# Kernel optimization log

Hardware: AMD Instinct MI355X
Metric: run time of the kernel (lower is better)

Reference implementation:

```python
import jax, jax.numpy as jnp
import numpy as np

VOCAB, BLOCK, C, H, L = 65, 60, 384, 6, 6
HS = C // H  # 64
EPS = 1e-5


def _ln(x, g, b):
    mu = jnp.mean(x, axis=-1, keepdims=True)
    var = jnp.mean(jnp.square(x - mu), axis=-1, keepdims=True)
    return (x - mu) * jax.lax.rsqrt(var + EPS) * g + b


def setup_inputs() -> dict:
    key = jax.random.key(0)
    ks = jax.random.split(key, 16)
    std = 0.02
    B, T = 2048, 60
    inp = {
        'context': jax.random.randint(ks[0], (B, T), 0, VOCAB),
        'tok_emb': std * jax.random.normal(ks[1], (VOCAB, C), jnp.float32),
        'pos_emb': std * jax.random.normal(ks[2], (BLOCK, C), jnp.float32),
        # per-head projections stacked: [L, H, C, HS]
        'wq': std * jax.random.normal(ks[3], (L, H, C, HS), jnp.float32),
        'wk': std * jax.random.normal(ks[4], (L, H, C, HS), jnp.float32),
        'wv': std * jax.random.normal(ks[5], (L, H, C, HS), jnp.float32),
        'wo': std * jax.random.normal(ks[6], (L, C, C), jnp.float32),
        'bo': jnp.zeros((L, C), jnp.float32),
        'ln1_g': jnp.ones((L, C), jnp.float32),
        'ln1_b': jnp.zeros((L, C), jnp.float32),
        'ln2_g': jnp.ones((L, C), jnp.float32),
        'ln2_b': jnp.zeros((L, C), jnp.float32),
        'w1': std * jax.random.normal(ks[7], (L, C, 4 * C), jnp.float32),
        'b1': jnp.zeros((L, 4 * C), jnp.float32),
        'w2': std * jax.random.normal(ks[8], (L, 4 * C, C), jnp.float32),
        'b2': jnp.zeros((L, C), jnp.float32),
        'lnf_g': jnp.ones((C,), jnp.float32),
        'lnf_b': jnp.zeros((C,), jnp.float32),
        'lm_w': std * jax.random.normal(ks[9], (C, VOCAB), jnp.float32),
        'lm_b': jnp.zeros((VOCAB,), jnp.float32),
    }
    return inp


def _forward(context, tok_emb, pos_emb, wq, wk, wv, wo, bo,
             ln1_g, ln1_b, ln2_g, ln2_b, w1, b1, w2, b2,
             lnf_g, lnf_b, lm_w, lm_b):
    B, T = context.shape
    x = tok_emb[context] + pos_emb[:T]  # [B,T,C]
    causal = jnp.tril(jnp.ones((T, T), bool))
    neg_inf = jnp.finfo(x.dtype).min

    def block(x, p):
        (wq_l, wk_l, wv_l, wo_l, bo_l, g1, b1n, g2, b2n, w1_l, bb1, w2_l, bb2) = p
        h = _ln(x, g1, b1n)
        q = jnp.einsum('btc,hcd->bhtd', h, wq_l)
        k = jnp.einsum('btc,hcd->bhtd', h, wk_l)
        v = jnp.einsum('btc,hcd->bhtd', h, wv_l)
        scores = jnp.einsum('bhtd,bhsd->bhts', q, k) * (HS ** -0.5)
        scores = jnp.where(causal, scores, neg_inf)
        probs = jax.nn.softmax(scores, axis=-1)
        o = jnp.einsum('bhts,bhsd->bhtd', probs, v)
        o = o.transpose(0, 2, 1, 3).reshape(B, T, C)  # concat heads
        x = x + o @ wo_l + bo_l
        h = _ln(x, g2, b2n)
        x = x + jax.nn.relu(h @ w1_l + bb1) @ w2_l + bb2
        return x, None

    params = (wq, wk, wv, wo, bo, ln1_g, ln1_b, ln2_g, ln2_b, w1, b1, w2, b2)
    x, _ = jax.lax.scan(block, x, params)
    x = _ln(x, lnf_g, lnf_b)
    return x @ lm_w + lm_b  # [B,T,VOCAB]


def reference(context, tok_emb, pos_emb, wq, wk, wv, wo, bo,
              ln1_g, ln1_b, ln2_g, ln2_b, w1, b1, w2, b2,
              lnf_g, lnf_b, lm_w, lm_b):
    return _forward(context, tok_emb, pos_emb, wq, wk, wv, wo, bo,
                    ln1_g, ln1_b, ln2_g, ln2_b, w1, b1, w2, b2,
                    lnf_g, lnf_b, lm_w, lm_b)
```

## Files before the change

### kernel.cpp

```cpp
#include <hip/hip_runtime.h>


#define B_  2048
#define T_  60
#define C_  384
#define H_  6
#define HS_ 64
#define L_  6
#define FF_ 1536
#define V_  65

typedef unsigned int  u32;
typedef unsigned short u16;
typedef short bf16x8 __attribute__((ext_vector_type(8)));
typedef float f32x4  __attribute__((ext_vector_type(4)));

__device__ __forceinline__ float bf2f(u32 u) {
  return __uint_as_float(u << 16);
}
__device__ __forceinline__ u16 f2bf(float f) {
  u32 u = __float_as_uint(f);
  u = u + 0x7FFFu + ((u >> 16) & 1u);
  return (u16)(u >> 16);
}

typedef const __attribute__((address_space(1))) unsigned int gas_u32;
typedef __attribute__((address_space(3))) unsigned int las_u32;
__device__ __forceinline__ void gload16(const u16* g, u16* l) {
  __builtin_amdgcn_global_load_lds((gas_u32*)g, (las_u32*)l, 16, 0, 0);
}

__global__ void tconv_k(const float* __restrict__ src, u16* __restrict__ dst,
                        int K, int N, long srcStride, int nH, long sL, long sH)
{
  __shared__ float t[32][33];
  int z = blockIdx.z;
  int l = z / nH, hh = z % nH;
  const float* s = src + (long)z * srcStride;
  u16* d = dst + l * sL + hh * sH;
  int n0 = blockIdx.x * 32, k0 = blockIdx.y * 32;
  for (int yy = threadIdx.y; yy < 32; yy += 8) {
    int k = k0 + yy, n = n0 + threadIdx.x;
    t[yy][threadIdx.x] = (k < K && n < N) ? s[(long)k * N + n] : 0.f;
  }
  __syncthreads();
  for (int yy = threadIdx.y; yy < 32; yy += 8) {
    int n = n0 + yy, k = k0 + threadIdx.x;
    if (n < N && k < K) d[(long)n * K + k] = f2bf(t[threadIdx.x][yy]);
  }
}

__global__ __launch_bounds__(256) void embed_k(const int* __restrict__ ctx,
    const float* __restrict__ tok, const float* __restrict__ pos,
    float* __restrict__ x)
{
  int idx = blockIdx.x * 256 + threadIdx.x;
  int row = idx / (C_ / 4);
  int c   = (idx % (C_ / 4)) * 4;
  int t   = row % T_;
  int tk  = ctx[row];
  float4 a = *(const float4*)(tok + (long)tk * C_ + c);
  float4 p = *(const float4*)(pos + (long)t  * C_ + c);
  float4 o = make_float4(a.x + p.x, a.y + p.y, a.z + p.z, a.w + p.w);
  *(float4*)(x + (long)idx * 4) = o;
}

__global__ __launch_bounds__(256) void ln_k(const float* __restrict__ x,
    const float* __restrict__ g, const float* __restrict__ b,
    u16* __restrict__ h)
{
  int lane = threadIdx.x & 63;
  int wv   = threadIdx.x >> 6;
  long row = (long)blockIdx.x * 4 + wv;
  const float* xr = x + row * C_;
  int c0 = lane * 6;
  float v0[6];
  #pragma unroll
  for (int i = 0; i < 6; i++) v0[i] = xr[c0 + i];
  float s = 0.f, sq = 0.f;
  #pragma unroll
  for (int i = 0; i < 6; i++) { s += v0[i]; sq += v0[i] * v0[i]; }
  #pragma unroll
  for (int off = 32; off > 0; off >>= 1) {
    s  += __shfl_xor(s,  off, 64);
    sq += __shfl_xor(sq, off, 64);
  }
  float mu  = s * (1.f / C_);
  float var = sq * (1.f / C_) - mu * mu;
  float rs  = rsqrtf(var + 1e-5f);
  u16* hr = h + row * C_;
  #pragma unroll
  for (int i = 0; i < 6; i++) {
    float hv = (v0[i] - mu) * rs * g[c0 + i] + b[c0 + i];
    hr[c0 + i] = f2bf(hv);
  }
}

template<int RELU, int RES, int OBF>
__global__ __launch_bounds__(512) void gemm128g(const u16* __restrict__ A,
    const u16* __restrict__ Wt, const float* __restrict__ bias,
    const float* __restrict__ resid, void* __restrict__ outp,
    int N, int K, int mT, int nT)
{
  __shared__ __align__(16) u16 As[2][128][4][8];
  __shared__ __align__(16) u16 Bs[2][128][4][8];
  int tid = threadIdx.x;
  int bid = blockIdx.x;
  int mtile, ntile;
  if ((mT & 7) == 0) {
    int xcd = bid & 7, loc = bid >> 3;
    int q = loc / nT;
    mtile = xcd * (mT >> 3) + q;
    ntile = loc - q * nT;
  } else {
    int q = bid / nT;
    mtile = q;
    ntile = bid - q * nT;
  }
  long mBase = (long)mtile * 128;
  int  nBase = ntile * 128;
  int lane = tid & 63, wv = tid >> 6;
  int l15 = lane & 15, l4 = lane >> 4;
  int wr = wv >> 1, wc = wv & 1;
  int srow = tid >> 2;
  int seg  = (tid & 3) ^ ((tid >> 4) & 3);
  const u16* aL = A  + (mBase + srow) * (long)K + seg * 8;
  const u16* bL = Wt + ((long)nBase + srow) * K + seg * 8;
  u16* aD0 = &As[0][wv << 4][0][0];
  u16* bD0 = &Bs[0][wv << 4][0][0];
  u16* aD1 = &As[1][wv << 4][0][0];
  u16* bD1 = &Bs[1][wv << 4][0][0];
  int swR = l4 ^ (l15 >> 2);

  f32x4 acc[2][4];
  #pragma unroll
  for (int i = 0; i < 2; i++)
    #pragma unroll
    for (int j = 0; j < 4; j++)
      acc[i][j] = (f32x4){0.f, 0.f, 0.f, 0.f};

  gload16(aL, aD0);
  gload16(bL, bD0);
  __syncthreads();

  int cur = 0;
  for (int k0 = 0; k0 < K; k0 += 32) {
    if (k0 + 32 < K) {
      gload16(aL + k0 + 32, cur ? aD0 : aD1);
      gload16(bL + k0 + 32, cur ? bD0 : bD1);
    }
    bf16x8 af[2], bfr[4];
    #pragma unroll
    for (int i = 0; i < 2; i++)
      af[i] = *(const bf16x8*)&As[cur][wr * 32 + i * 16 + l15][swR][0];
    #pragma unroll
    for (int j = 0; j < 4; j++)
      bfr[j] = *(const bf16x8*)&Bs[cur][wc * 64 + j * 16 + l15][swR][0];
    #pragma unroll
    for (int i = 0; i < 2; i++)
      #pragma unroll
      for (int j = 0; j < 4; j++)
        acc[i][j] = __builtin_amdgcn_mfma_f32_16x16x32_bf16(
            af[i], bfr[j], acc[i][j], 0, 0, 0);
    __syncthreads();
    cur ^= 1;
  }

  #pragma unroll
  for (int i = 0; i < 2; i++) {
    #pragma unroll
    for (int j = 0; j < 4; j++) {
      int n = nBase + wc * 64 + j * 16 + l15;
      float bv = bias ? bias[n] : 0.f;
      #pragma unroll
      for (int r = 0; r < 4; r++) {
        long row = mBase + wr * 32 + i * 16 + l4 * 4 + r;
        float vv = acc[i][j][r] + bv;
        if (RELU) vv = fmaxf(vv, 0.f);
        if (RES)  vv += resid[row * N + n];
        if (OBF) ((u16*)outp)[row * N + n] = f2bf(vv);
        else     ((float*)outp)[row * N + n] = vv;
      }
    }
  }
}

template<int OBF>
__global__ __launch_bounds__(256) void gemm_head(const u16* __restrict__ A,
    const u16* __restrict__ Wt, const float* __restrict__ bias,
    void* __restrict__ outp, int N, int K)
{
  __shared__ __align__(16) u16 As[128][4][8];
  __shared__ __align__(16) u16 Bs[64][4][8];
  int tid  = threadIdx.x;
  int nt   = blockIdx.x;
  int nBase = nt * 64;
  long mBase = (long)blockIdx.y * 128;
  int lane = tid & 63, wv = tid >> 6;
  int l15 = lane & 15, l4 = lane >> 4;
  int sseg = tid & 3;
  int srow = tid >> 2;
  int swW = sseg ^ ((srow >> 2) & 3);
  int swR = l4 ^ (l15 >> 2);
  const u16* a0p = A + (mBase + srow) * K + sseg * 8;
  const u16* a1p = a0p + (long)64 * K;
  bool colOK = (nBase + srow) < N;
  const u16* bp  = Wt + (long)(nBase + srow) * K + sseg * 8;

  f32x4 acc[2][4];
  #pragma unroll
  for (int i = 0; i < 2; i++)
    #pragma unroll
    for (int j = 0; j < 4; j++)
      acc[i][j] = (f32x4){0.f, 0.f, 0.f, 0.f};

  for (int k0 = 0; k0 < K; k0 += 32) {
    uint4 av0 = *(const uint4*)(a0p + k0);
    uint4 av1 = *(const uint4*)(a1p + k0);
    uint4 bv  = colOK ? *(const uint4*)(bp + k0) : make_uint4(0, 0, 0, 0);
    *(uint4*)&As[srow][swW][0]      = av0;
    *(uint4*)&As[srow + 64][swW][0] = av1;
    *(uint4*)&Bs[srow][swW][0]      = bv;
    __syncthreads();
    bf16x8 af[2], bfr[4];
    af[0] = *(const bf16x8*)&As[wv * 32 + l15][swR][0];
    af[1] = *(const bf16x8*)&As[wv * 32 + 16 + l15][swR][0];
    #pragma unroll
    for (int j = 0; j < 4; j++)
      bfr[j] = *(const bf16x8*)&Bs[j * 16 + l15][swR][0];
    #pragma unroll
    for (int i = 0; i < 2; i++)
      #pragma unroll
      for (int j = 0; j < 4; j++)
        acc[i][j] = __builtin_amdgcn_mfma_f32_16x16x32_bf16(
            af[i], bfr[j], acc[i][j], 0, 0, 0);
    __syncthreads();
  }

  #pragma unroll
  for (int i = 0; i < 2; i++) {
    #pragma unroll
    for (int j = 0; j < 4; j++) {
      int n = nBase + j * 16 + l15;
      if (n < N) {
        #pragma unroll
        for (int r = 0; r < 4; r++) {
          long row = mBase + wv * 32 + i * 16 + l4 * 4 + r;
          float vv = acc[i][j][r];
          if (bias) vv += bias[n];
          if (OBF) ((u16*)outp)[row * N + n] = f2bf(vv);
          else     ((float*)outp)[row * N + n] = vv;
        }
      }
    }
  }
}

__global__ __launch_bounds__(256) void attn_k(const u16* __restrict__ qkv,
    u16* __restrict__ ao)
{
  __shared__ __align__(16) u16 qs[64][72];
  __shared__ __align__(16) u16 ks[64][72];
  __shared__ __align__(16) u16 vT[64][72];
  __shared__ __align__(16) u16 ps[64][72];
  int tid = threadIdx.x;
  int bb = blockIdx.x / H_;
  int hh = blockIdx.x % H_;
  const u16* base = qkv + ((long)bb * T_) * 1152 + hh * HS_;

  for (int i = tid; i < 576; i += 256)
    ((uint4*)vT)[i] = make_uint4(0, 0, 0, 0);
  __syncthreads();

  for (int i = tid; i < 480; i += 256) {
    int t = i >> 3, d0 = (i & 7) << 3;
    const u16* rp = base + (long)t * 1152;
    *(uint4*)&qs[t][d0] = *(const uint4*)(rp + d0);
    *(uint4*)&ks[t][d0] = *(const uint4*)(rp + 384 + d0);
    uint4 rv = *(const uint4*)(rp + 768 + d0);
    u16 vv[8] = {(u16)(rv.x & 0xffffu), (u16)(rv.x >> 16),
                 (u16)(rv.y & 0xffffu), (u16)(rv.y >> 16),
                 (u16)(rv.z & 0xffffu), (u16)(rv.z >> 16),
                 (u16)(rv.w & 0xffffu), (u16)(rv.w >> 16)};
    #pragma unroll
    for (int m = 0; m < 8; m++) vT[d0 + m][t] = vv[m];
  }
  __syncthreads();

  int lane = tid & 63, wv = tid >> 6;
  int l15 = lane & 15, quad = lane >> 4;

  bf16x8 aq0 = *(const bf16x8*)&qs[wv * 16 + l15][quad * 8];
  bf16x8 aq1 = *(const bf16x8*)&qs[wv * 16 + l15][32 + quad * 8];
  f32x4 s[4];
  #pragma unroll
  for (int jt = 0; jt < 4; jt++) {
    bf16x8 b0 = *(const bf16x8*)&ks[jt * 16 + l15][quad * 8];
    bf16x8 b1 = *(const bf16x8*)&ks[jt * 16 + l15][32 + quad * 8];
    f32x4 a2 = (f32x4){0.f, 0.f, 0.f, 0.f};
    a2 = __builtin_amdgcn_mfma_f32_16x16x32_bf16(aq0, b0, a2, 0, 0, 0);
    a2 = __builtin_amdgcn_mfma_f32_16x16x32_bf16(aq1, b1, a2, 0, 0, 0);
    s[jt] = a2;
  }

  int rbase = wv * 16 + quad * 4;
  #pragma unroll
  for (int r = 0; r < 4; r++) {
    int row = rbase + r;
    float v0[4];
    #pragma unroll
    for (int jt = 0; jt < 4; jt++) {
      int col = jt * 16 + l15;
      float sv = s[jt][r] * 0.125f;
      v0[jt] = (col <= row) ? sv : -1e30f;
    }
    float m = fmaxf(fmaxf(v0[0], v0[1]), fmaxf(v0[2], v0[3]));
    #pragma unroll
    for (int off = 1; off < 16; off <<= 1) m = fmaxf(m, __shfl_xor(m, off, 64));
    float sum = 0.f;
    #pragma unroll
    for (int jt = 0; jt < 4; jt++) { v0[jt] = __expf(v0[jt] - m); sum += v0[jt]; }
    #pragma unroll
    for (int off = 1; off < 16; off <<= 1) sum += __shfl_xor(sum, off, 64);
    float inv = 1.f / sum;
    #pragma unroll
    for (int jt = 0; jt < 4; jt++)
      ps[row][jt * 16 + l15] = f2bf(v0[jt] * inv);
  }
  __syncthreads();

  bf16x8 ap0 = *(const bf16x8*)&ps[wv * 16 + l15][quad * 8];
  bf16x8 ap1 = *(const bf16x8*)&ps[wv * 16 + l15][32 + quad * 8];
  long obase = ((long)bb * T_) * C_ + hh * HS_;
  #pragma unroll
  for (int dt = 0; dt < 4; dt++) {
    bf16x8 b0 = *(const bf16x8*)&vT[dt * 16 + l15][quad * 8];
    bf16x8 b1 = *(const bf16x8*)&vT[dt * 16 + l15][32 + quad * 8];
    f32x4 a2 = (f32x4){0.f, 0.f, 0.f, 0.f};
    a2 = __builtin_amdgcn_mfma_f32_16x16x32_bf16(ap0, b0, a2, 0, 0, 0);
    a2 = __builtin_amdgcn_mfma_f32_16x16x32_bf16(ap1, b1, a2, 0, 0, 0);
    #pragma unroll
    for (int r = 0; r < 4; r++) {
      int row = rbase + r;
      if (row < T_)
        ao[obase + (long)row * C_ + dt * 16 + l15] = f2bf(a2[r]);
    }
  }
}

extern "C" void kernel_launch(void* const* d_in, const int* in_sizes, int n_in,
                              void* d_out, int out_size, void* d_ws, size_t ws_size,
                              hipStream_t stream)
{
  const int*   ctx  = (const int*)  d_in[0];
  const float* tok  = (const float*)d_in[1];
  const float* pos  = (const float*)d_in[2];
  const float* wq   = (const float*)d_in[3];
  const float* wk   = (const float*)d_in[4];
  const float* wv   = (const float*)d_in[5];
  const float* wo   = (const float*)d_in[6];
  const float* bo   = (const float*)d_in[7];
  const float* ln1g = (const float*)d_in[8];
  const float* ln1b = (const float*)d_in[9];
  const float* ln2g = (const float*)d_in[10];
  const float* ln2b = (const float*)d_in[11];
  const float* w1   = (const float*)d_in[12];
  const float* b1   = (const float*)d_in[13];
  const float* w2   = (const float*)d_in[14];
  const float* b2   = (const float*)d_in[15];
  const float* lnfg = (const float*)d_in[16];
  const float* lnfb = (const float*)d_in[17];
  const float* lmw  = (const float*)d_in[18];
  const float* lmb  = (const float*)d_in[19];
  float* out = (float*)d_out;

  const long nQKV = (long)L_ * H_ * C_ * HS_;
  const long nWO  = (long)L_ * C_ * C_;
  const long nW1  = (long)L_ * C_ * FF_;
  const long nLM  = (long)C_ * V_;
  u16* wqkvT = (u16*)d_ws;
  u16* woT = wqkvT + 3 * nQKV;
  u16* w1T = woT + nWO;
  u16* w2T = w1T + nW1;
  u16* lmT = w2T + nW1;
  const size_t wbytes = (size_t)(nQKV * 3 + nWO + nW1 * 2 + nLM) * 2;

  int chunkB = 32;
  {
    const int cand[] = {256, 128, 64, 32};
    for (int i = 0; i < 4; i++) {
      size_t U = (size_t)cand[i] * T_ * C_ * 2;
      if (wbytes + 7 * U <= ws_size) { chunkB = cand[i]; break; }
    }
  }
  const long BTc = (long)chunkB * T_;
  char* wsb = (char*)d_ws + wbytes;
  const size_t U = (size_t)BTc * C_ * 2;
  float* x    = (float*)wsb;
  u16*   h    = (u16*)(wsb + 2 * U);
  char*  reg  = wsb + 3 * U;
  u16* qkvb = (u16*)reg;
  u16* ab   = (u16*)(reg + 3 * U);
  u16* fb   = (u16*)reg;

  {
    dim3 tb(32, 8);
    const long sL = 1152L * 384, sH = 64L * 384, sec = 384L * 384;
    tconv_k<<<dim3(2, 12, L_ * H_), tb, 0, stream>>>(wq, wqkvT,
        C_, HS_, (long)C_ * HS_, H_, sL, sH);
    tconv_k<<<dim3(2, 12, L_ * H_), tb, 0, stream>>>(wk, wqkvT + sec,
        C_, HS_, (long)C_ * HS_, H_, sL, sH);
    tconv_k<<<dim3(2, 12, L_ * H_), tb, 0, stream>>>(wv, wqkvT + 2 * sec,
        C_, HS_, (long)C_ * HS_, H_, sL, sH);
    tconv_k<<<dim3(12, 12, L_), tb, 0, stream>>>(wo, woT,
        C_, C_, (long)C_ * C_, 1, (long)C_ * C_, 0);
    tconv_k<<<dim3(48, 12, L_), tb, 0, stream>>>(w1, w1T,
        C_, FF_, (long)C_ * FF_, 1, (long)C_ * FF_, 0);
    tconv_k<<<dim3(12, 48, L_), tb, 0, stream>>>(w2, w2T,
        FF_, C_, (long)FF_ * C_, 1, (long)FF_ * C_, 0);
    tconv_k<<<dim3(3, 12, 1), tb, 0, stream>>>(lmw, lmT,
        C_, V_, (long)C_ * V_, 1, 0, 0);
  }

  const long qkvL = 1152L * 384;
  const long woL  = (long)C_ * C_;
  const long w1L  = (long)C_ * FF_;
  dim3 blk(256);
  dim3 blk5(512);
  dim3 gEmb((u32)(BTc * C_ / 4 / 256));
  dim3 gLN((u32)(BTc / 4));
  int mT = (int)(BTc / 128);
  dim3 gHd(2, (u32)(BTc / 128));
  dim3 gAt((u32)(chunkB * H_));

  for (int c0 = 0; c0 < B_; c0 += chunkB) {
    const long tok0 = (long)c0 * T_;
    const int* ctxc = ctx + tok0;
    float* outc = out + tok0 * V_;

    embed_k<<<gEmb, blk, 0, stream>>>(ctxc, tok, pos, x);

    for (int l = 0; l < L_; l++) {
      ln_k<<<gLN, blk, 0, stream>>>(x, ln1g + l * C_, ln1b + l * C_, h);
      gemm128g<0,0,1><<<dim3(mT * 9), blk5, 0, stream>>>(h, wqkvT + l * qkvL,
          nullptr, nullptr, qkvb, 1152, C_, mT, 9);
      attn_k<<<gAt, blk, 0, stream>>>(qkvb, ab);
      gemm128g<0,1,0><<<dim3(mT * 3), blk5, 0, stream>>>(ab, woT + l * woL,
          bo + l * C_, x, x, C_, C_, mT, 3);
      ln_k<<<gLN, blk, 0, stream>>>(x, ln2g + l * C_, ln2b + l * C_, h);
      gemm128g<1,0,1><<<dim3(mT * 12), blk5, 0, stream>>>(h, w1T + l * w1L,
          b1 + l * FF_, nullptr, fb, FF_, C_, mT, 12);
      gemm128g<0,1,0><<<dim3(mT * 3), blk5, 0, stream>>>(fb, w2T + l * w1L,
          b2 + l * C_, x, x, C_, FF_, mT, 3);
    }

    ln_k<<<gLN, blk, 0, stream>>>(x, lnfg, lnfb, h);
    gemm_head<0><<<gHd, blk, 0, stream>>>(h, lmT, lmb, outc, V_, C_);
  }
}
```

Measured before the change: 6.752 ms.

## Fuse MLP up and down projections into one kernel keeping hidden tile in LDS

Adds a fused MLP kernel in which each 128-row block computes the 1536-wide ReLU hidden activations in 128-column chunks, stores each chunk as bf16 in LDS, and immediately accumulates the down-projection into a 128x384 register accumulator. This removes the global round trip of the FF intermediate and one kernel launch per layer. Buffers are rearranged so the workspace needs 6 units instead of 7, which allows chunk size 512 and therefore fewer chunk iterations. The costs are much lower grid parallelism (one block per 128 rows), large register and LDS use per block that limit occupancy, and a serialized two-phase pipeline inside each block.

```diff
diff --git a/kernel.cpp b/kernel.cpp
--- a/kernel.cpp
+++ b/kernel.cpp
@@ -29,6 +29,7 @@
 __device__ __forceinline__ void gload16(const u16* g, u16* l) {
   __builtin_amdgcn_global_load_lds((gas_u32*)g, (las_u32*)l, 16, 0, 0);
 }
+#define MFMA16(a, b, c) __builtin_amdgcn_mfma_f32_16x16x32_bf16((a), (b), (c), 0, 0, 0)
 
 __global__ void tconv_k(const float* __restrict__ src, u16* __restrict__ dst,
                         int K, int N, long srcStride, int nH, long sL, long sH)
@@ -180,6 +181,140 @@
         if (RES)  vv += resid[row * N + n];
         if (OBF) ((u16*)outp)[row * N + n] = f2bf(vv);
         else     ((float*)outp)[row * N + n] = vv;
+      }
+    }
+  }
+}
+
+__global__ __launch_bounds__(512) void mlp_fused(const u16* __restrict__ h,
+    const u16* __restrict__ W1t, const float* __restrict__ b1,
+    const u16* __restrict__ W2t, const float* __restrict__ b2,
+    float* __restrict__ x, int mT)
+{
+  __shared__ __align__(16) u16 lds[73728];
+  int tid = threadIdx.x;
+  int bid = blockIdx.x;
+  int mtile;
+  if ((mT & 7) == 0) {
+    int xcd = bid & 7, loc = bid >> 3;
+    mtile = xcd * (mT >> 3) + loc;
+  } else {
+    mtile = bid;
+  }
+  long mBase = (long)mtile * 128;
+  int lane = tid & 63, w = tid >> 6;
+  int l15 = lane & 15, l4 = lane >> 4;
+  int wrU = w >> 1, wcU = w & 1;
+  int wr2 = w >> 2, wc2 = w & 3;
+  int srow = tid >> 2;
+  int seg  = (tid & 3) ^ ((tid >> 4) & 3);
+  const u16* aL = h   + (mBase + srow) * 384 + seg * 8;
+  const u16* bU = W1t + (long)srow * 384 + seg * 8;
+  const u16* bD = W2t + (long)srow * 1536 + seg * 8;
+  int wvOff = w << 9;
+  int swR = l4 ^ (l15 >> 2);
+  int uaOff = (wrU * 32 + l15) * 32 + swR * 8;
+  int ubOff = (wcU * 64 + l15) * 32 + swR * 8;
+  int dbOff = (wc2 * 96 + l15) * 32 + swR * 8;
+
+  f32x4 accO[4][6];
+  #pragma unroll
+  for (int i = 0; i < 4; i++)
+    #pragma unroll
+    for (int j = 0; j < 6; j++)
+      accO[i][j] = (f32x4){0.f, 0.f, 0.f, 0.f};
+
+  for (int cc = 0; cc < 12; ++cc) {
+    const u16* bUc = bU + cc * 49152;
+    gload16(aL,  &lds[16384 + wvOff]);
+    gload16(bUc, &lds[32768 + wvOff]);
+    __syncthreads();
+    f32x4 accU[2][4];
+    #pragma unroll
+    for (int i = 0; i < 2; i++)
+      #pragma unroll
+      for (int j = 0; j < 4; j++)
+        accU[i][j] = (f32x4){0.f, 0.f, 0.f, 0.f};
+    int cur = 0;
+    for (int kt = 0; kt < 12; ++kt) {
+      int k0 = kt * 32;
+      if (kt < 11) {
+        gload16(aL  + k0 + 32, &lds[16384 + ((cur ^ 1) << 12) + wvOff]);
+        gload16(bUc + k0 + 32, &lds[32768 + ((cur ^ 1) << 12) + wvOff]);
+      }
+      bf16x8 af[2], bf[4];
+      #pragma unroll
+      for (int i = 0; i < 2; i++)
+        af[i] = *(const bf16x8*)&lds[16384 + (cur << 12) + uaOff + i * 512];
+      #pragma unroll
+      for (int j = 0; j < 4; j++)
+        bf[j] = *(const bf16x8*)&lds[32768 + (cur << 12) + ubOff + j * 512];
+      #pragma unroll
+      for (int i = 0; i < 2; i++)
+        #pragma unroll
+        for (int j = 0; j < 4; j++)
+          accU[i][j] = MFMA16(af[i], bf[j], accU[i][j]);
+      __syncthreads();
+      cur ^= 1;
+    }
+    #pragma unroll
+    for (int j = 0; j < 4; ++j) {
+      int col = wcU * 64 + j * 16 + l15;
+      float bv = b1[cc * 128 + col];
+      int chi = col >> 3, cpos = col & 7;
+      #pragma unroll
+      for (int i = 0; i < 2; ++i)
+        #pragma unroll
+        for (int r = 0; r < 4; ++r) {
+          int row = wrU * 32 + i * 16 + l4 * 4 + r;
+          float vv = fmaxf(accU[i][j][r] + bv, 0.f);
+          lds[row * 128 + ((chi ^ (l4 * 4 + r)) << 3) + cpos] = f2bf(vv);
+        }
+    }
+    const u16* bDc = bD + cc * 128;
+    gload16(bDc,          &lds[49152 + wvOff]);
+    gload16(bDc + 196608, &lds[49152 + 4096 + wvOff]);
+    gload16(bDc + 393216, &lds[49152 + 8192 + wvOff]);
+    __syncthreads();
+    int cd = 0;
+    for (int kk = 0; kk < 4; ++kk) {
+      if (kk < 3) {
+        const u16* s = bDc + (kk + 1) * 32;
+        int nb = 49152 + ((cd ^ 1) ? 12288 : 0);
+        gload16(s,          &lds[nb + wvOff]);
+        gload16(s + 196608, &lds[nb + 4096 + wvOff]);
+        gload16(s + 393216, &lds[nb + 8192 + wvOff]);
+      }
+      bf16x8 au[4], bw[6];
+      #pragma unroll
+      for (int i = 0; i < 4; ++i) {
+        int row = wr2 * 64 + i * 16 + l15;
+        au[i] = *(const bf16x8*)&lds[row * 128 + ((((kk << 2) + l4) ^ l15) << 3)];
+      }
+      #pragma unroll
+      for (int j = 0; j < 6; ++j)
+        bw[j] = *(const bf16x8*)&lds[49152 + (cd ? 12288 : 0) + dbOff + j * 512];
+      #pragma unroll
+      for (int i = 0; i < 4; ++i)
+        #pragma unroll
+        for (int j = 0; j < 6; ++j)
+          accO[i][j] = MFMA16(au[i], bw[j], accO[i][j]);
+      __syncthreads();
+      cd ^= 1;
+    }
+  }
+
+  #pragma unroll
+  for (int i = 0; i < 4; ++i) {
+    #pragma unroll
+    for (int j = 0; j < 6; ++j) {
+      int n = wc2 * 96 + j * 16 + l15;
+      float bv = b2[n];
+      #pragma unroll
+      for (int r = 0; r < 4; ++r) {
+        long row = mBase + wr2 * 64 + i * 16 + l4 * 4 + r;
+        long idx = row * 384 + n;
+        x[idx] = accO[i][j][r] + bv + x[idx];
       }
     }
   }
@@ -387,21 +522,18 @@
 
   int chunkB = 32;
   {
-    const int cand[] = {256, 128, 64, 32};
-    for (int i = 0; i < 4; i++) {
+    const int cand[] = {512, 256, 128, 64, 32};
+    for (int i = 0; i < 5; i++) {
       size_t U = (size_t)cand[i] * T_ * C_ * 2;
-      if (wbytes + 7 * U <= ws_size) { chunkB = cand[i]; break; }
+      if (wbytes + 6 * U <= ws_size) { chunkB = cand[i]; break; }
     }
   }
   const long BTc = (long)chunkB * T_;
   char* wsb = (char*)d_ws + wbytes;
   const size_t U = (size_t)BTc * C_ * 2;
   float* x    = (float*)wsb;
-  u16*   h    = (u16*)(wsb + 2 * U);
-  char*  reg  = wsb + 3 * U;
-  u16* qkvb = (u16*)reg;
-  u16* ab   = (u16*)(reg + 3 * U);
-  u16* fb   = (u16*)reg;
+  u16*   qkvb = (u16*)(wsb + 2 * U);
+  u16*   hab  = (u16*)(wsb + 5 * U);
 
   {
     dim3 tb(32, 8);
@@ -441,20 +573,18 @@
     embed_k<<<gEmb, blk, 0, stream>>>(ctxc, tok, pos, x);
 
     for (int l = 0; l < L_; l++) {
-      ln_k<<<gLN, blk, 0, stream>>>(x, ln1g + l * C_, ln1b + l * C_, h);
-      gemm128g<0,0,1><<<dim3(mT * 9), blk5, 0, stream>>>(h, wqkvT + l * qkvL,
+      ln_k<<<gLN, blk, 0, stream>>>(x, ln1g + l * C_, ln1b + l * C_, hab);
+      gemm128g<0,0,1><<<dim3(mT * 9), blk5, 0, stream>>>(hab, wqkvT + l * qkvL,
           nullptr, nullptr, qkvb, 1152, C_, mT, 9);
-      attn_k<<<gAt, blk, 0, stream>>>(qkvb, ab);
-      gemm128g<0,1,0><<<dim3(mT * 3), blk5, 0, stream>>>(ab, woT + l * woL,
+      attn_k<<<gAt, blk, 0, stream>>>(qkvb, hab);
+      gemm128g<0,1,0><<<dim3(mT * 3), blk5, 0, stream>>>(hab, woT + l * woL,
           bo + l * C_, x, x, C_, C_, mT, 3);
-      ln_k<<<gLN, blk, 0, stream>>>(x, ln2g + l * C_, ln2b + l * C_, h);
-      gemm128g<1,0,1><<<dim3(mT * 12), blk5, 0, stream>>>(h, w1T + l * w1L,
-          b1 + l * FF_, nullptr, fb, FF_, C_, mT, 12);
-      gemm128g<0,1,0><<<dim3(mT * 3), blk5, 0, stream>>>(fb, w2T + l * w1L,
-          b2 + l * C_, x, x, C_, FF_, mT, 3);
-    }
-
-    ln_k<<<gLN, blk, 0, stream>>>(x, lnfg, lnfb, h);
-    gemm_head<0><<<gHd, blk, 0, stream>>>(h, lmT, lmb, outc, V_, C_);
-  }
-}
+      ln_k<<<gLN, blk, 0, stream>>>(x, ln2g + l * C_, ln2b + l * C_, hab);
+      mlp_fused<<<dim3(mT), blk5, 0, stream>>>(hab, w1T + l * w1L,
+          b1 + l * FF_, w2T + l * w1L, b2 + l * C_, x, mT);
+    }
+
+    ln_k<<<gLN, blk, 0, stream>>>(x, lnfg, lnfb, hab);
+    gemm_head<0><<<gHd, blk, 0, stream>>>(hab, lmT, lmb, outc, V_, C_);
+  }
+}
```

Result: faster. 5.893 ms (-12.7%).
